# Optimization experiments

Measured on AMD Instinct MI355X. Metric: run time of the kernel, lower is better.

## Reference

```python
import jax, jax.numpy as jnp
import numpy as np

PATCH_SIZE = 3
CHANNELS = 1
SIGMA_RAW = 0.5
SIGMA_EFF = SIGMA_RAW * PATCH_SIZE ** 2  # sigma * patch_size**2 as in __init__


def setup_inputs() -> dict:
    key = jax.random.key(0)
    kx, ky = jax.random.split(key)
    N, C, H, W = 64, CHANNELS, 64, 64
    x = jax.random.normal(kx, (N, C, H, W), dtype=jnp.float32)
    y = jax.random.normal(ky, (N, C, H, W), dtype=jnp.float32)
    return {"x": x, "y": y}


def _pairwise_patch_distance(A, B):
    # A: (N_A, C, H, W), B: (N_B, C, H, W)
    N_A, C, H, W = A.shape
    N_B = B.shape[0]
    # broadcast pairwise squared pixel diffs: (N_A, N_B, C, H, W)
    pixel_diff = (A[:, None] - B[None]) ** 2
    kern = jnp.ones((1, C, PATCH_SIZE, PATCH_SIZE), dtype=A.dtype)  # OIHW
    d = jax.lax.conv_general_dilated(
        pixel_diff.reshape(N_A * N_B, C, H, W), kern,
        window_strides=(1, 1), padding='VALID',
        dimension_numbers=('NCHW', 'OIHW', 'NCHW'))
    H_new, W_new = d.shape[-2], d.shape[-1]
    return d.reshape(N_A, N_B, H_new, W_new)


def _gaussian_kernel(D):
    return jnp.exp(-D / (2.0 * SIGMA_EFF ** 2))


def _off_mean(K):
    # K: (N, N, h, w); mean over all off-diagonal (i != j) entries
    N, _, h, w = K.shape
    mask = ~jnp.eye(N, dtype=bool)
    total = jnp.sum(jnp.where(mask[:, :, None, None], K, jnp.zeros((), K.dtype)))
    count = (N * (N - 1)) * h * w
    return total / count


def reference(x, y):
    K_xx = _gaussian_kernel(_pairwise_patch_distance(x, x))
    K_xy = _gaussian_kernel(_pairwise_patch_distance(x, y))
    K_yy = _gaussian_kernel(_pairwise_patch_distance(y, y))
    return _off_mean(K_xx) - 2.0 * jnp.mean(K_xy) + _off_mean(K_yy)
```

## Files before the change

### kernel.cpp

```cpp
#include <hip/hip_runtime.h>


typedef __attribute__((ext_vector_type(8))) short short8v;
typedef __attribute__((ext_vector_type(4))) float f32x4;

#define NPOS 3844
#define WSTR 26

#if __has_builtin(__builtin_amdgcn_exp2f)
#define EXP2F(v) __builtin_amdgcn_exp2f(v)
#else
#define EXP2F(v) __expf((v) * 0.69314718055994530942f)
#endif

template<int CTRL>
__device__ __forceinline__ float dpp0_f(float v) {
    int r = __builtin_amdgcn_update_dpp(0, __float_as_int(v), CTRL, 0xf, 0xf, true);
    return __int_as_float(r);
}
template<int CTRL, int RM>
__device__ __forceinline__ float dppm_f(float v) {
    int r = __builtin_amdgcn_update_dpp(0, __float_as_int(v), CTRL, RM, 0xf, true);
    return __int_as_float(r);
}
__device__ __forceinline__ float wave_reduce_f(float v) {
    v += dpp0_f<0x111>(v);
    v += dpp0_f<0x112>(v);
    v += dpp0_f<0x114>(v);
    v += dpp0_f<0x118>(v);
    v += dppm_f<0x142, 0xa>(v);
    v += dppm_f<0x143, 0xc>(v);
    return v;
}
__device__ __forceinline__ unsigned int bf16rne(float f) {
    unsigned int u = __float_as_uint(f);
    return (u + 0x7fffu + ((u >> 16) & 1u)) >> 16;
}

__global__ __launch_bounds__(256) void mmd_fused_kernel(
    const float* __restrict__ x, const float* __restrict__ y,
    float* __restrict__ part)
{
    const int t = threadIdx.x, wid = t >> 6, lane = t & 63;
    const int p  = blockIdx.x >> 4;
    const int qg = blockIdx.x & 15;
    const int q  = qg * 4 + wid;

    __shared__ unsigned short win[128 * WSTR];
    __shared__ unsigned short rec[4 * 128 * 8];
    __shared__ unsigned short rec8[4 * 128];
    __shared__ float pre[4][128];

    {
        const int cg1 = (qg < 15) ? qg + 1 : 15;
        #pragma unroll
        for (int k = 0; k < 3; ++k) {
            int it = t + k * 256;
            int n = it / 6, rem = it % 6;
            int u = rem >> 1, cg = rem & 1;
            const float* img = (n < 64) ? (x + n * 4096) : (y + (n - 64) * 4096);
            float4 v = *reinterpret_cast<const float4*>(
                img + (p + u) * 64 + ((cg ? cg1 : qg) << 2));
            unsigned int d0 = bf16rne(v.x) | (bf16rne(v.y) << 16);
            unsigned int d1 = bf16rne(v.z) | (bf16rne(v.w) << 16);
            unsigned int* w32 = reinterpret_cast<unsigned int*>(
                &win[n * WSTR + u * 8 + cg * 4]);
            w32[0] = d0; w32[1] = d1;
        }
    }
    __syncthreads();

    #pragma unroll
    for (int k = 0; k < 2; ++k) {
        int rid = t + k * 256;
        int ql = rid >> 7, n = rid & 127;
        const unsigned short* wp = &win[n * WSTR + ql];
        unsigned short b[9];
        #pragma unroll
        for (int u = 0; u < 3; ++u) {
            b[u * 3 + 0] = wp[u * 8 + 0];
            b[u * 3 + 1] = wp[u * 8 + 1];
            b[u * 3 + 2] = wp[u * 8 + 2];
        }
        uint4 pk;
        pk.x = b[0] | ((unsigned)b[1] << 16);
        pk.y = b[2] | ((unsigned)b[3] << 16);
        pk.z = b[4] | ((unsigned)b[5] << 16);
        pk.w = b[6] | ((unsigned)b[7] << 16);
        *reinterpret_cast<uint4*>(&rec[(size_t)rid * 8]) = pk;
        rec8[rid] = b[8];
    }
    __syncthreads();

    const int r = lane & 15, kg = lane >> 4;
    short8v frag[8];
    #pragma unroll
    for (int g = 0; g < 8; ++g) {
        short8v f = {0, 0, 0, 0, 0, 0, 0, 0};
        if (kg == 0)
            f = *reinterpret_cast<const short8v*>(&rec[(size_t)(wid * 128 + g * 16 + r) * 8]);
        else if (kg == 1)
            f[0] = (short)rec8[wid * 128 + g * 16 + r];
        frag[g] = f;
    }

    const float NS   = -1.0f / (40.5f * 0.69314718055994530942f);
    const float M2NS = -2.0f * NS;
    const f32x4 zf = {0.f, 0.f, 0.f, 0.f};

    f32x4 accd[8];
    #pragma unroll
    for (int g = 0; g < 8; ++g)
        accd[g] = __builtin_amdgcn_mfma_f32_16x16x32_bf16(frag[g], frag[g], zf, 0, 0, 0);

    const bool holder = ((lane >> 2) & 3) == kg;
    #pragma unroll
    for (int g = 0; g < 8; ++g) {
        float lo = (lane & 1) ? accd[g][1] : accd[g][0];
        float hi = (lane & 1) ? accd[g][3] : accd[g][2];
        float v  = (lane & 2) ? hi : lo;
        if (holder) pre[wid][g * 16 + (lane & 15)] = NS * v;
    }
    __syncthreads();

    float pa[8][4], pb[8];
    #pragma unroll
    for (int g = 0; g < 8; ++g) {
        const float* pp = &pre[wid][g * 16 + kg * 4];
        pa[g][0] = pp[0]; pa[g][1] = pp[1]; pa[g][2] = pp[2]; pa[g][3] = pp[3];
        pb[g] = pre[wid][g * 16 + (lane & 15)];
    }

    float acc_diag = 0.f, acc_same = 0.f, acc_cross = 0.f;

    #pragma unroll
    for (int g = 0; g < 8; ++g)
        #pragma unroll
        for (int m = 0; m < 4; ++m)
            acc_diag += EXP2F(fmaf(accd[g][m], M2NS, pa[g][m] + pb[g]));

    #pragma unroll
    for (int ti = 1; ti < 8; ++ti)
        #pragma unroll
        for (int tj = 0; tj < ti; ++tj) {
            f32x4 c4 = __builtin_amdgcn_mfma_f32_16x16x32_bf16(frag[ti], frag[tj], zf, 0, 0, 0);
            float e = 0.f;
            #pragma unroll
            for (int m = 0; m < 4; ++m)
                e += EXP2F(fmaf(c4[m], M2NS, pa[ti][m] + pb[tj]));
            if (ti >= 4 && tj < 4) acc_cross += e; else acc_same += e;
        }

    acc_diag  = wave_reduce_f(acc_diag);
    acc_same  = wave_reduce_f(acc_same);
    acc_cross = wave_reduce_f(acc_cross);
    if (lane == 63 && q < 62) {
        const int pid = p * 62 + q;
        part[pid]        = acc_diag;
        part[4096 + pid] = acc_same;
        part[8192 + pid] = acc_cross;
    }
}

__global__ __launch_bounds__(1024) void mmd_final_kernel(
    const float* __restrict__ part, float* __restrict__ out)
{
    const int t = threadIdx.x;
    double sd = 0.0, ss = 0.0, sc = 0.0;
    for (int e = t; e < NPOS; e += 1024) {
        sd += (double)part[e];
        ss += (double)part[4096 + e];
        sc += (double)part[8192 + e];
    }
    #pragma unroll
    for (int off = 32; off > 0; off >>= 1) {
        sd += __shfl_xor(sd, off);
        ss += __shfl_xor(ss, off);
        sc += __shfl_xor(sc, off);
    }
    __shared__ double w[3][16];
    const int lane = t & 63, wd = t >> 6;
    if (lane == 0) { w[0][wd] = sd; w[1][wd] = ss; w[2][wd] = sc; }
    __syncthreads();
    if (t == 0) {
        double Sd = 0.0, Ss = 0.0, Sc = 0.0;
        #pragma unroll
        for (int k = 0; k < 16; ++k) { Sd += w[0][k]; Ss += w[1][k]; Sc += w[2][k]; }
        double S_off = (Sd - 128.0 * (double)NPOS) + 2.0 * Ss;
        const double cnt_off = 64.0 * 63.0 * 62.0 * 62.0;
        const double cnt_all = 64.0 * 64.0 * 62.0 * 62.0;
        out[0] = (float)(S_off / cnt_off - 2.0 * Sc / cnt_all);
    }
}

extern "C" void kernel_launch(void* const* d_in, const int* in_sizes, int n_in,
                              void* d_out, int out_size, void* d_ws, size_t ws_size,
                              hipStream_t stream) {
    const float* x = (const float*)d_in[0];
    const float* y = (const float*)d_in[1];
    float* out  = (float*)d_out;
    float* part = (float*)d_ws;

    mmd_fused_kernel<<<62 * 16, 256, 0, stream>>>(x, y, part);
    mmd_final_kernel<<<1, 1024, 0, stream>>>(part, out);
}
```

Baseline: 20.28 us.

## Precompute patch norms in scalar pass, reduce per block, shrink final kernel

Computes each patch's squared norm with scalar FMAs while building the record, which removes a syncthreads and the separate norm-extraction pass from the first MFMA results. The diagonal MFMA is now interleaved with its exp, and split accumulators shorten the add dependency chains. Block-level partial sums go to shared memory and are written once per block, so the final kernel reduces 992 values with 256 threads instead of 3844 with 1024. It also sets launch bounds to 4 blocks per CU. Norms are now taken from the bf16-rounded values with scalar FMAs, so they may differ slightly from the MFMA-computed ones.

```diff
diff --git a/kernel.cpp b/kernel.cpp
--- a/kernel.cpp
+++ b/kernel.cpp
@@ -6,6 +6,7 @@
 
 #define NPOS 3844
 #define WSTR 26
+#define NBLK 992
 
 #if __has_builtin(__builtin_amdgcn_exp2f)
 #define EXP2F(v) __builtin_amdgcn_exp2f(v)
@@ -37,7 +38,7 @@
     return (u + 0x7fffu + ((u >> 16) & 1u)) >> 16;
 }
 
-__global__ __launch_bounds__(256) void mmd_fused_kernel(
+__global__ __launch_bounds__(256, 4) void mmd_fused_kernel(
     const float* __restrict__ x, const float* __restrict__ y,
     float* __restrict__ part)
 {
@@ -49,7 +50,11 @@
     __shared__ unsigned short win[128 * WSTR];
     __shared__ unsigned short rec[4 * 128 * 8];
     __shared__ unsigned short rec8[4 * 128];
-    __shared__ float pre[4][128];
+    __shared__ float pren[4 * 128];
+    __shared__ float wred[3][4];
+
+    const float NS   = -1.0f / (40.5f * 0.69314718055994530942f);
+    const float M2NS = -2.0f * NS;
 
     {
         const int cg1 = (qg < 15) ? qg + 1 : 15;
@@ -82,6 +87,12 @@
             b[u * 3 + 1] = wp[u * 8 + 1];
             b[u * 3 + 2] = wp[u * 8 + 2];
         }
+        float pre = 0.f;
+        #pragma unroll
+        for (int e = 0; e < 9; ++e) {
+            float fv = __uint_as_float((unsigned)b[e] << 16);
+            pre = fmaf(fv, fv, pre);
+        }
         uint4 pk;
         pk.x = b[0] | ((unsigned)b[1] << 16);
         pk.y = b[2] | ((unsigned)b[3] << 16);
@@ -89,6 +100,7 @@
         pk.w = b[6] | ((unsigned)b[7] << 16);
         *reinterpret_cast<uint4*>(&rec[(size_t)rid * 8]) = pk;
         rec8[rid] = b[8];
+        pren[rid] = pre * NS;
     }
     __syncthreads();
 
@@ -103,41 +115,26 @@
             f[0] = (short)rec8[wid * 128 + g * 16 + r];
         frag[g] = f;
     }
-
-    const float NS   = -1.0f / (40.5f * 0.69314718055994530942f);
-    const float M2NS = -2.0f * NS;
+    float pa[8][4], pb[8];
+    #pragma unroll
+    for (int g = 0; g < 8; ++g) {
+        const float* pp = &pren[wid * 128 + g * 16 + kg * 4];
+        pa[g][0] = pp[0]; pa[g][1] = pp[1]; pa[g][2] = pp[2]; pa[g][3] = pp[3];
+        pb[g] = pren[wid * 128 + g * 16 + r];
+    }
+
     const f32x4 zf = {0.f, 0.f, 0.f, 0.f};
-
-    f32x4 accd[8];
-    #pragma unroll
-    for (int g = 0; g < 8; ++g)
-        accd[g] = __builtin_amdgcn_mfma_f32_16x16x32_bf16(frag[g], frag[g], zf, 0, 0, 0);
-
-    const bool holder = ((lane >> 2) & 3) == kg;
+    float ad0 = 0.f, ad1 = 0.f, as0 = 0.f, as1 = 0.f, ac0 = 0.f, ac1 = 0.f;
+
     #pragma unroll
     for (int g = 0; g < 8; ++g) {
-        float lo = (lane & 1) ? accd[g][1] : accd[g][0];
-        float hi = (lane & 1) ? accd[g][3] : accd[g][2];
-        float v  = (lane & 2) ? hi : lo;
-        if (holder) pre[wid][g * 16 + (lane & 15)] = NS * v;
-    }
-    __syncthreads();
-
-    float pa[8][4], pb[8];
-    #pragma unroll
-    for (int g = 0; g < 8; ++g) {
-        const float* pp = &pre[wid][g * 16 + kg * 4];
-        pa[g][0] = pp[0]; pa[g][1] = pp[1]; pa[g][2] = pp[2]; pa[g][3] = pp[3];
-        pb[g] = pre[wid][g * 16 + (lane & 15)];
-    }
-
-    float acc_diag = 0.f, acc_same = 0.f, acc_cross = 0.f;
-
-    #pragma unroll
-    for (int g = 0; g < 8; ++g)
+        f32x4 c4 = __builtin_amdgcn_mfma_f32_16x16x32_bf16(frag[g], frag[g], zf, 0, 0, 0);
+        float e = 0.f;
         #pragma unroll
         for (int m = 0; m < 4; ++m)
-            acc_diag += EXP2F(fmaf(accd[g][m], M2NS, pa[g][m] + pb[g]));
+            e += EXP2F(fmaf(c4[m], M2NS, pa[g][m] + pb[g]));
+        if (g & 1) ad1 += e; else ad0 += e;
+    }
 
     #pragma unroll
     for (int ti = 1; ti < 8; ++ti)
@@ -148,29 +145,41 @@
             #pragma unroll
             for (int m = 0; m < 4; ++m)
                 e += EXP2F(fmaf(c4[m], M2NS, pa[ti][m] + pb[tj]));
-            if (ti >= 4 && tj < 4) acc_cross += e; else acc_same += e;
-        }
-
-    acc_diag  = wave_reduce_f(acc_diag);
-    acc_same  = wave_reduce_f(acc_same);
-    acc_cross = wave_reduce_f(acc_cross);
-    if (lane == 63 && q < 62) {
-        const int pid = p * 62 + q;
-        part[pid]        = acc_diag;
-        part[4096 + pid] = acc_same;
-        part[8192 + pid] = acc_cross;
-    }
-}
-
-__global__ __launch_bounds__(1024) void mmd_final_kernel(
+            if (ti >= 4 && tj < 4) { if (tj & 1) ac1 += e; else ac0 += e; }
+            else                   { if (tj & 1) as1 += e; else as0 += e; }
+        }
+
+    float acc_diag  = wave_reduce_f(ad0 + ad1);
+    float acc_same  = wave_reduce_f(as0 + as1);
+    float acc_cross = wave_reduce_f(ac0 + ac1);
+    if (lane == 63) {
+        const bool valid = (q < 62);
+        wred[0][wid] = valid ? acc_diag  : 0.f;
+        wred[1][wid] = valid ? acc_same  : 0.f;
+        wred[2][wid] = valid ? acc_cross : 0.f;
+    }
+    __syncthreads();
+    if (t == 0) {
+        #pragma unroll
+        for (int c = 0; c < 3; ++c)
+            part[c * NBLK + blockIdx.x] =
+                (wred[c][0] + wred[c][1]) + (wred[c][2] + wred[c][3]);
+    }
+}
+
+__global__ __launch_bounds__(256) void mmd_final_kernel(
     const float* __restrict__ part, float* __restrict__ out)
 {
     const int t = threadIdx.x;
     double sd = 0.0, ss = 0.0, sc = 0.0;
-    for (int e = t; e < NPOS; e += 1024) {
-        sd += (double)part[e];
-        ss += (double)part[4096 + e];
-        sc += (double)part[8192 + e];
+    #pragma unroll
+    for (int k = 0; k < 4; ++k) {
+        int e = t + k * 256;
+        if (e < NBLK) {
+            sd += (double)part[e];
+            ss += (double)part[NBLK + e];
+            sc += (double)part[2 * NBLK + e];
+        }
     }
     #pragma unroll
     for (int off = 32; off > 0; off >>= 1) {
@@ -178,14 +187,14 @@
         ss += __shfl_xor(ss, off);
         sc += __shfl_xor(sc, off);
     }
-    __shared__ double w[3][16];
+    __shared__ double w[3][4];
     const int lane = t & 63, wd = t >> 6;
     if (lane == 0) { w[0][wd] = sd; w[1][wd] = ss; w[2][wd] = sc; }
     __syncthreads();
     if (t == 0) {
-        double Sd = 0.0, Ss = 0.0, Sc = 0.0;
-        #pragma unroll
-        for (int k = 0; k < 16; ++k) { Sd += w[0][k]; Ss += w[1][k]; Sc += w[2][k]; }
+        double Sd = w[0][0] + w[0][1] + w[0][2] + w[0][3];
+        double Ss = w[1][0] + w[1][1] + w[1][2] + w[1][3];
+        double Sc = w[2][0] + w[2][1] + w[2][2] + w[2][3];
         double S_off = (Sd - 128.0 * (double)NPOS) + 2.0 * Ss;
         const double cnt_off = 64.0 * 63.0 * 62.0 * 62.0;
         const double cnt_all = 64.0 * 64.0 * 62.0 * 62.0;
@@ -202,5 +211,5 @@
     float* part = (float*)d_ws;
 
     mmd_fused_kernel<<<62 * 16, 256, 0, stream>>>(x, y, part);
-    mmd_final_kernel<<<1, 1024, 0, stream>>>(part, out);
-}
+    mmd_final_kernel<<<1, 256, 0, stream>>>(part, out);
+}
```

After: 18.01 us. -11.2%, faster.
